# Performance work log

Hardware: AMD Instinct MI355X
Metric: run time of the kernel (lower is better)

Reference implementation:

```python
import jax, jax.numpy as jnp
import numpy as np

P = 3            # spline degree
N_KNOTS = 68     # len(t); K = N_KNOTS - P - 1 = 64
B, D_IN, D_OUT = 4096, 256, 256


def bspline_basis(u, t, p):
    """Vectorized Cox-de Boor recursion.
    u: (N,) evaluation points; t: (n,) sorted knot vector.
    Returns (N, n - p - 1) basis matrix.
    """
    n = t.shape[0]
    uu = u[:, None]                                   # (N, 1)
    # degree-0 indicators over half-open knot intervals: (N, n-1)
    Bmat = ((uu >= t[None, :-1]) & (uu < t[None, 1:])).astype(u.dtype)
    for d in range(1, p + 1):
        ld = t[d:n - 1] - t[:n - d - 1]               # (n-d-1,) left denominators
        rd = t[d + 1:] - t[1:n - d]                   # (n-d-1,) right denominators
        lt = jnp.where(ld > 0, (uu - t[None, :n - d - 1]) / jnp.where(ld > 0, ld, 1.0), 0.0)
        rt = jnp.where(rd > 0, (t[None, d + 1:] - uu) / jnp.where(rd > 0, rd, 1.0), 0.0)
        Bmat = lt * Bmat[:, :-1] + rt * Bmat[:, 1:]
    return Bmat                                        # (N, K)


def setup_inputs() -> dict:
    key = jax.random.key(0)
    k1, k2 = jax.random.split(key)
    K = N_KNOTS - P - 1
    x = jax.random.normal(k1, (B, D_IN), dtype=jnp.float32)
    coeffs = 0.01 * jax.random.normal(k2, (D_OUT, D_IN, K), dtype=jnp.float32)
    mask = jnp.ones((D_OUT, D_IN), dtype=jnp.float32)
    t = jnp.linspace(-4.0, 4.0, N_KNOTS, dtype=jnp.float32)
    return {"x": x, "coeffs": coeffs, "mask": mask, "t": t}


def reference(x, coeffs, mask, t):
    b, d_in = x.shape
    # basis for all (batch, input-dim) points at once -> (B, d_in, K)
    Bx = bspline_basis(x.reshape(-1), t, P).reshape(b, d_in, -1)
    C = coeffs * mask[..., None]                      # (d_out, d_in, K)
    y = jnp.einsum('bik,oik->bo', Bx, C)              # (B, d_out)
    return y
```

## Files before the change

### kernel.cpp

```cpp
#include <hip/hip_runtime.h>

#define NKNOTS 68
#define B_     4096
#define DIN    256
#define DOUT   256
#define KB_    64
#define BM     128
#define BN     128
#define LDA    80
#define KSPLIT 16
#define IPS    (DIN / KSPLIT)

typedef unsigned short ushort_t;
typedef unsigned long long u64_t;
typedef float   f32x4    __attribute__((ext_vector_type(4)));
typedef unsigned int u32x4 __attribute__((ext_vector_type(4)));
typedef ushort_t us16x4  __attribute__((ext_vector_type(4)));
typedef int     int4v    __attribute__((ext_vector_type(4)));

typedef __attribute__((address_space(1))) const unsigned int gu32;
typedef __attribute__((address_space(3))) unsigned int lu32;

__device__ __forceinline__ float bf2f(ushort_t b) {
    union { unsigned u; float f; } c; c.u = ((unsigned)b) << 16; return c.f;
}
__device__ __forceinline__ ushort_t f2bf(float f) {
    union { float f; unsigned u; } c; c.f = f;
    unsigned u = c.u;
    return (ushort_t)((u + 0x7FFFu + ((u >> 16) & 1u)) >> 16);
}
__device__ __forceinline__ bool is_fp32(const void* tkn) {
    return ((*(const unsigned*)tkn) & 0xFFFFu) == 0u;
}

__global__ void kan_prep1(const void* __restrict__ coeffs,
                          const void* __restrict__ mask,
                          const void* __restrict__ x,
                          const void* __restrict__ tkn,
                          unsigned* __restrict__ smax,
                          u64_t* __restrict__ rec64) {
    __shared__ float tt[NKNOTS];
    __shared__ float wmax[4];
    int blk = blockIdx.x;
    int lt  = threadIdx.x;
    bool f32 = is_fp32(tkn);

    if (blk < 2048) {
        int tid = blk * 256 + lt;
        int oi = tid >> 3;
        int o  = tid >> 11;
        int k8 = (tid & 7) * 8;
        size_t base = (size_t)oi * KB_ + k8;
        float v[8], m;
        if (f32) {
            const float* cf = (const float*)coeffs + base;
            f32x4 a = *(const f32x4*)cf;
            f32x4 b = *(const f32x4*)(cf + 4);
            v[0]=a.x; v[1]=a.y; v[2]=a.z; v[3]=a.w; v[4]=b.x; v[5]=b.y; v[6]=b.z; v[7]=b.w;
            m = ((const float*)mask)[oi];
        } else {
            const ushort_t* ch = (const ushort_t*)coeffs + base;
            u32x4 w = *(const u32x4*)ch;
            const ushort_t* h = (const ushort_t*)&w;
            #pragma unroll
            for (int e = 0; e < 8; ++e) v[e] = bf2f(h[e]);
            m = bf2f(((const ushort_t*)mask)[oi]);
        }
        float mx = 0.f;
        #pragma unroll
        for (int e = 0; e < 8; ++e) mx = fmaxf(mx, fabsf(v[e] * m));
        #pragma unroll
        for (int off = 32; off >= 1; off >>= 1)
            mx = fmaxf(mx, __shfl_down(mx, off, 64));
        if ((lt & 63) == 0) wmax[lt >> 6] = mx;
        __syncthreads();
        if (lt == 0) {
            float M = fmaxf(fmaxf(wmax[0], wmax[1]), fmaxf(wmax[2], wmax[3]));
            atomicMax(smax + o, __float_as_uint(M));
        }
    } else {
        if (lt < NKNOTS) tt[lt] = f32 ? ((const float*)tkn)[lt] : bf2f(((const ushort_t*)tkn)[lt]);
        __syncthreads();
        int g = (blk - 2048) * 256 + lt;
        float u = f32 ? ((const float*)x)[g] : bf2f(((const ushort_t*)x)[g]);
        float N0 = 0.f, N1 = 0.f, N2 = 0.f, N3 = 0.f;
        int j = 0;
        bool valid = (u >= tt[0]) && (u < tt[NKNOTS - 1]);
        if (valid) {
            int lo = 0, hi = NKNOTS - 1;
            #pragma unroll
            for (int it = 0; it < 7; ++it) {
                int mid = (lo + hi) >> 1;
                if (u < tt[mid]) hi = mid; else lo = mid;
            }
            j = lo;
            float Nv[4];
            Nv[0] = 1.f; Nv[1] = 0.f; Nv[2] = 0.f; Nv[3] = 0.f;
            #pragma unroll
            for (int d = 1; d <= 3; ++d) {
                float saved = 0.f;
                #pragma unroll
                for (int r = 0; r < 3; ++r) {
                    if (r < d) {
                        int il = j + r + 1 - d;
                        int ir = j + r + 1;
                        il = il < 0 ? 0 : (il > 67 ? 67 : il);
                        ir = ir > 67 ? 67 : ir;
                        float tl = tt[il], tr = tt[ir];
                        float denom = tr - tl;
                        float temp = (denom > 0.f) ? Nv[r] / denom : 0.f;
                        Nv[r] = saved + (tr - u) * temp;
                        saved = (u - tl) * temp;
                    }
                }
                Nv[d] = saved;
            }
            N0 = Nv[0]; N1 = Nv[1]; N2 = Nv[2]; N3 = Nv[3];
        }
        int s = j - 3;
        int sc = s < 0 ? 0 : (s > 60 ? 60 : s);
        unsigned pack = 0;
        #pragma unroll
        for (int r = 0; r < 4; ++r) {
            int rr = (sc + r) - s;
            float v = 0.f;
            v = (rr == 0) ? N0 : v;
            v = (rr == 1) ? N1 : v;
            v = (rr == 2) ? N2 : v;
            v = (rr == 3) ? N3 : v;
            int q = __float2int_rn(127.0f * v);
            pack |= ((unsigned)(q & 0xFF)) << (8 * r);
        }
        rec64[g] = ((u64_t)(unsigned)sc << 32) | pack;
    }
}

__global__ void kan_prep2(const void* __restrict__ coeffs,
                          const void* __restrict__ mask,
                          const void* __restrict__ tkn,
                          const unsigned* __restrict__ smax,
                          signed char* __restrict__ cp8) {
    int tid = blockIdx.x * 256 + threadIdx.x;
    int oi = tid >> 3;
    int o  = tid >> 11;
    int k8 = (tid & 7) * 8;
    size_t base = (size_t)oi * KB_ + k8;
    bool f32 = is_fp32(tkn);
    float maxv = __uint_as_float(smax[o]);
    float sinv = (maxv > 0.f) ? (127.0f / maxv) : 0.f;
    float v[8], m;
    if (f32) {
        const float* cf = (const float*)coeffs + base;
        f32x4 a = *(const f32x4*)cf;
        f32x4 b = *(const f32x4*)(cf + 4);
        v[0]=a.x; v[1]=a.y; v[2]=a.z; v[3]=a.w; v[4]=b.x; v[5]=b.y; v[6]=b.z; v[7]=b.w;
        m = ((const float*)mask)[oi];
    } else {
        const ushort_t* ch = (const ushort_t*)coeffs + base;
        u32x4 w = *(const u32x4*)ch;
        const ushort_t* h = (const ushort_t*)&w;
        #pragma unroll
        for (int e = 0; e < 8; ++e) v[e] = bf2f(h[e]);
        m = bf2f(((const ushort_t*)mask)[oi]);
    }
    u64_t pk = 0;
    #pragma unroll
    for (int e = 0; e < 8; ++e) {
        int q = __float2int_rn(v[e] * m * sinv);
        pk |= ((u64_t)((unsigned)q & 0xFF)) << (8 * e);
    }
    *(u64_t*)(cp8 + base) = pk;
}

__global__ __launch_bounds__(256, 4) void kan_gemm(
    const signed char* __restrict__ cp8,
    const u64_t* __restrict__ rec64,
    const unsigned* __restrict__ smax,
    ushort_t* __restrict__ part)
{
    __shared__ __align__(16) unsigned char As[BM * LDA];
    __shared__ __align__(16) unsigned char Bs[2][BN * KB_];

    int t  = threadIdx.x;
    int bx = blockIdx.x;
    int kt = bx & (KSPLIT - 1);
    int mt = (bx >> 4) & 31;
    int nt = bx >> 9;
    int b0 = mt * BM;
    int o0 = nt * BN;
    int i0 = kt * IPS;

    int wave = t >> 6;
    int lane = t & 63;
    int wm = (wave & 1) * 64;
    int wn = (wave >> 1) * 64;
    int l15 = lane & 15;
    int l4  = lane >> 4;

    #define STAGE(i_, p_)                                                                 \
        {                                                                                 \
            _Pragma("unroll")                                                             \
            for (int j = 0; j < 2; ++j) {                                                 \
                int slot = wave * 128 + j * 64 + lane;                                    \
                int row  = slot >> 2;                                                     \
                int c    = slot & 3;                                                      \
                const signed char* g = cp8 + ((size_t)(o0 + row) * DIN + (i_)) * KB_ + c * 16; \
                lu32* l = (lu32*)(&Bs[p_][(wave * 128 + j * 64) * 16]);                   \
                __builtin_amdgcn_global_load_lds((gu32*)g, l, 16, 0, 0);                  \
            }                                                                             \
        }

    {
        unsigned* As32 = (unsigned*)As;
        #pragma unroll
        for (int j = 0; j < (BM * LDA / 4) / 256; ++j) As32[t + j * 256] = 0u;
    }

    int zrow = t >> 2;
    int zq   = t & 3;
    size_t gb0 = (size_t)(b0 + zrow) * DIN;
    size_t gb1 = (size_t)(b0 + zrow + 64) * DIN;

    STAGE(i0, 0);
    u64_t cur_r0 = rec64[gb0 + i0];
    u64_t cur_r1 = rec64[gb1 + i0];

    int4v acc[4][4];
    #pragma unroll
    for (int a = 0; a < 4; ++a)
        #pragma unroll
        for (int b = 0; b < 4; ++b)
            acc[a][b] = (int4v){0, 0, 0, 0};

    __syncthreads();

    int last0 = 0, last1 = 0;
    u64_t nxt_r0 = 0, nxt_r1 = 0;
    for (int ii = 0; ii < IPS; ++ii) {
        int p = ii & 1;
        int s0 = (int)((cur_r0 >> 32) & 0xFF);
        int s1 = (int)((cur_r1 >> 32) & 0xFF);
        unsigned char v0 = (unsigned char)((cur_r0 >> (8 * zq)) & 0xFF);
        unsigned char v1 = (unsigned char)((cur_r1 >> (8 * zq)) & 0xFF);
        As[zrow * LDA + last0 + zq] = 0;
        As[(zrow + 64) * LDA + last1 + zq] = 0;
        As[zrow * LDA + s0 + zq] = v0;
        As[(zrow + 64) * LDA + s1 + zq] = v1;
        last0 = s0; last1 = s1;
        __syncthreads();
        if (ii + 1 < IPS) {
            int i1 = i0 + ii + 1;
            STAGE(i1, p ^ 1);
            nxt_r0 = rec64[gb0 + i1];
            nxt_r1 = rec64[gb1 + i1];
        }
        int4v af[4], bfr[4];
        #pragma unroll
        for (int a = 0; a < 4; ++a)
            af[a] = *(const int4v*)(&As[(wm + a * 16 + l15) * LDA + l4 * 16]);
        #pragma unroll
        for (int b = 0; b < 4; ++b)
            bfr[b] = *(const int4v*)(&Bs[p][(wn + b * 16 + l15) * KB_ + l4 * 16]);
        #pragma unroll
        for (int a = 0; a < 4; ++a)
            #pragma unroll
            for (int b = 0; b < 4; ++b)
                acc[a][b] = __builtin_amdgcn_mfma_i32_16x16x64_i8(af[a], bfr[b], acc[a][b], 0, 0, 0);
        cur_r0 = nxt_r0; cur_r1 = nxt_r1;
        __syncthreads();
    }

    ushort_t* pout = part + (size_t)kt * (B_ * DOUT);
    float sb[4];
    #pragma unroll
    for (int b = 0; b < 4; ++b) {
        int col = o0 + wn + b * 16 + l15;
        sb[b] = __uint_as_float(smax[col]) * (1.0f / (127.0f * 127.0f));
    }
    #pragma unroll
    for (int a = 0; a < 4; ++a) {
        int row_base = b0 + wm + a * 16 + l4 * 4;
        #pragma unroll
        for (int b = 0; b < 4; ++b) {
            int col = o0 + wn + b * 16 + l15;
            #pragma unroll
            for (int e = 0; e < 4; ++e)
                pout[(size_t)(row_base + e) * DOUT + col] = f2bf((float)acc[a][b][e] * sb[b]);
        }
    }
    #undef STAGE
}

__global__ void kan_reduce(const ushort_t* __restrict__ part,
                           const void* __restrict__ tkn,
                           void* __restrict__ out) {
    int g = blockIdx.x * 256 + threadIdx.x;
    const us16x4* p4 = (const us16x4*)part;
    f32x4 s = (f32x4){0.f, 0.f, 0.f, 0.f};
    #pragma unroll
    for (int kt = 0; kt < KSPLIT; ++kt) {
        us16x4 v = p4[(size_t)kt * (B_ * DOUT / 4) + g];
        s.x += bf2f(v[0]); s.y += bf2f(v[1]); s.z += bf2f(v[2]); s.w += bf2f(v[3]);
    }
    if (is_fp32(tkn)) {
        ((f32x4*)out)[g] = s;
    } else {
        us16x4 o;
        o[0] = f2bf(s.x); o[1] = f2bf(s.y); o[2] = f2bf(s.z); o[3] = f2bf(s.w);
        ((us16x4*)out)[g] = o;
    }
}

extern "C" void kernel_launch(void* const* d_in, const int* in_sizes, int n_in,
                              void* d_out, int out_size, void* d_ws, size_t ws_size,
                              hipStream_t stream) {
    const void* x      = d_in[0];
    const void* coeffs = d_in[1];
    const void* mask   = d_in[2];
    const void* tkn    = d_in[3];

    char* ws = (char*)d_ws;
    signed char* cp8   = (signed char*)(ws);
    u64_t*       rec64 = (u64_t*)(ws + (4u  << 20));
    unsigned*    smax  = (unsigned*)(ws + (12u << 20));
    ushort_t*    part  = (ushort_t*)(ws + (13u << 20));

    hipMemsetAsync(smax, 0, 256 * sizeof(unsigned), stream);
    kan_prep1<<<6144, 256, 0, stream>>>(coeffs, mask, x, tkn, smax, rec64);
    kan_prep2<<<2048, 256, 0, stream>>>(coeffs, mask, tkn, smax, cp8);
    kan_gemm<<<1024, 256, 0, stream>>>(cp8, rec64, smax, part);
    kan_reduce<<<1024, 256, 0, stream>>>(part, tkn, d_out);
}
```

Measured before the change: 121.3 us.

## Halve GEMM K-split, process two input slices per step, drop atomic max

The GEMM now uses 8 K-splits instead of 16, and each block loads two input-dimension slices per pipeline step. This halves the partial-sum buffer written by the GEMM and read by the reduce kernel. B tiles in LDS get a padded stride to reduce bank conflicts, and the rec64 loads are vectorized to fetch two slices at once. The per-output max is no longer built with atomicMax on a memset buffer; each block writes its own max and consumers fold 8 entries. This removes the memset launch and the atomics, at the cost of 512 larger blocks with lower occupancy.

```diff
diff --git a/kernel.cpp b/kernel.cpp
--- a/kernel.cpp
+++ b/kernel.cpp
@@ -7,11 +7,14 @@
 #define KB_    64
 #define BM     128
 #define BN     128
-#define LDA    80
-#define KSPLIT 16
-#define IPS    (DIN / KSPLIT)
+#define LDA    144
+#define LDB    80
+#define KSPLIT 8
+#define IPS    32
+#define NSTEP  16
 
 typedef unsigned short ushort_t;
+typedef unsigned char uchar_t;
 typedef unsigned long long u64_t;
 typedef float   f32x4    __attribute__((ext_vector_type(4)));
 typedef unsigned int u32x4 __attribute__((ext_vector_type(4)));
@@ -37,7 +40,7 @@
                           const void* __restrict__ mask,
                           const void* __restrict__ x,
                           const void* __restrict__ tkn,
-                          unsigned* __restrict__ smax,
+                          float* __restrict__ smax64,
                           u64_t* __restrict__ rec64) {
     __shared__ float tt[NKNOTS];
     __shared__ float wmax[4];
@@ -48,7 +51,6 @@
     if (blk < 2048) {
         int tid = blk * 256 + lt;
         int oi = tid >> 3;
-        int o  = tid >> 11;
         int k8 = (tid & 7) * 8;
         size_t base = (size_t)oi * KB_ + k8;
         float v[8], m;
@@ -74,10 +76,8 @@
             mx = fmaxf(mx, __shfl_down(mx, off, 64));
         if ((lt & 63) == 0) wmax[lt >> 6] = mx;
         __syncthreads();
-        if (lt == 0) {
-            float M = fmaxf(fmaxf(wmax[0], wmax[1]), fmaxf(wmax[2], wmax[3]));
-            atomicMax(smax + o, __float_as_uint(M));
-        }
+        if (lt == 0)
+            smax64[blk] = fmaxf(fmaxf(wmax[0], wmax[1]), fmaxf(wmax[2], wmax[3]));
     } else {
         if (lt < NKNOTS) tt[lt] = f32 ? ((const float*)tkn)[lt] : bf2f(((const ushort_t*)tkn)[lt]);
         __syncthreads();
@@ -138,7 +138,7 @@
 __global__ void kan_prep2(const void* __restrict__ coeffs,
                           const void* __restrict__ mask,
                           const void* __restrict__ tkn,
-                          const unsigned* __restrict__ smax,
+                          const float* __restrict__ smax64,
                           signed char* __restrict__ cp8) {
     int tid = blockIdx.x * 256 + threadIdx.x;
     int oi = tid >> 3;
@@ -146,7 +146,9 @@
     int k8 = (tid & 7) * 8;
     size_t base = (size_t)oi * KB_ + k8;
     bool f32 = is_fp32(tkn);
-    float maxv = __uint_as_float(smax[o]);
+    float maxv = 0.f;
+    #pragma unroll
+    for (int e = 0; e < 8; ++e) maxv = fmaxf(maxv, smax64[(o << 3) + e]);
     float sinv = (maxv > 0.f) ? (127.0f / maxv) : 0.f;
     float v[8], m;
     if (f32) {
@@ -172,20 +174,20 @@
     *(u64_t*)(cp8 + base) = pk;
 }
 
-__global__ __launch_bounds__(256, 4) void kan_gemm(
+__global__ __launch_bounds__(256, 2) void kan_gemm(
     const signed char* __restrict__ cp8,
     const u64_t* __restrict__ rec64,
-    const unsigned* __restrict__ smax,
+    const float* __restrict__ smax64,
     ushort_t* __restrict__ part)
 {
-    __shared__ __align__(16) unsigned char As[BM * LDA];
-    __shared__ __align__(16) unsigned char Bs[2][BN * KB_];
+    __shared__ __align__(16) uchar_t As[BM * LDA];
+    __shared__ __align__(16) uchar_t Bs[2][2 * BN * LDB];
 
     int t  = threadIdx.x;
     int bx = blockIdx.x;
     int kt = bx & (KSPLIT - 1);
-    int mt = (bx >> 4) & 31;
-    int nt = bx >> 9;
+    int mt = (bx >> 3) & 31;
+    int nt = bx >> 8;
     int b0 = mt * BM;
     int o0 = nt * BN;
     int i0 = kt * IPS;
@@ -197,17 +199,27 @@
     int l15 = lane & 15;
     int l4  = lane >> 4;
 
-    #define STAGE(i_, p_)                                                                 \
-        {                                                                                 \
-            _Pragma("unroll")                                                             \
-            for (int j = 0; j < 2; ++j) {                                                 \
-                int slot = wave * 128 + j * 64 + lane;                                    \
-                int row  = slot >> 2;                                                     \
-                int c    = slot & 3;                                                      \
-                const signed char* g = cp8 + ((size_t)(o0 + row) * DIN + (i_)) * KB_ + c * 16; \
-                lu32* l = (lu32*)(&Bs[p_][(wave * 128 + j * 64) * 16]);                   \
-                __builtin_amdgcn_global_load_lds((gu32*)g, l, 16, 0, 0);                  \
-            }                                                                             \
+    size_t gsrc_base[5];
+    unsigned ldsoff[5];
+    #pragma unroll
+    for (int j = 0; j < 5; ++j) {
+        int slot = wave * 320 + j * 64 + lane;
+        int isl  = slot / 640;
+        int w640 = slot - isl * 640;
+        int row  = w640 / 5;
+        int c    = w640 - row * 5;
+        int cc   = (c > 3) ? 3 : c;
+        gsrc_base[j] = ((size_t)(o0 + row) * DIN + isl) * KB_ + cc * 16;
+        ldsoff[j] = (unsigned)((wave * 320 + j * 64) * 16);
+    }
+    #define STAGE(i_, p_)                                                              \
+        {                                                                              \
+            _Pragma("unroll")                                                          \
+            for (int j = 0; j < 5; ++j) {                                              \
+                const signed char* g = cp8 + gsrc_base[j] + (size_t)(i_) * KB_;        \
+                lu32* l = (lu32*)(&Bs[p_][ldsoff[j]]);                                 \
+                __builtin_amdgcn_global_load_lds((gu32*)g, l, 16, 0, 0);               \
+            }                                                                          \
         }
 
     {
@@ -222,8 +234,13 @@
     size_t gb1 = (size_t)(b0 + zrow + 64) * DIN;
 
     STAGE(i0, 0);
-    u64_t cur_r0 = rec64[gb0 + i0];
-    u64_t cur_r1 = rec64[gb1 + i0];
+    u64_t cur_r0[2], cur_r1[2];
+    {
+        u32x4 p0 = *(const u32x4*)(&rec64[gb0 + i0]);
+        u32x4 p1 = *(const u32x4*)(&rec64[gb1 + i0]);
+        cur_r0[0] = ((u64_t)p0.y << 32) | p0.x; cur_r0[1] = ((u64_t)p0.w << 32) | p0.z;
+        cur_r1[0] = ((u64_t)p1.y << 32) | p1.x; cur_r1[1] = ((u64_t)p1.w << 32) | p1.z;
+    }
 
     int4v acc[4][4];
     #pragma unroll
@@ -234,39 +251,50 @@
 
     __syncthreads();
 
-    int last0 = 0, last1 = 0;
-    u64_t nxt_r0 = 0, nxt_r1 = 0;
-    for (int ii = 0; ii < IPS; ++ii) {
-        int p = ii & 1;
-        int s0 = (int)((cur_r0 >> 32) & 0xFF);
-        int s1 = (int)((cur_r1 >> 32) & 0xFF);
-        unsigned char v0 = (unsigned char)((cur_r0 >> (8 * zq)) & 0xFF);
-        unsigned char v1 = (unsigned char)((cur_r1 >> (8 * zq)) & 0xFF);
-        As[zrow * LDA + last0 + zq] = 0;
-        As[(zrow + 64) * LDA + last1 + zq] = 0;
-        As[zrow * LDA + s0 + zq] = v0;
-        As[(zrow + 64) * LDA + s1 + zq] = v1;
-        last0 = s0; last1 = s1;
+    int last0[2] = {0, 0}, last1[2] = {0, 0};
+    u64_t nxt_r0[2] = {0, 0}, nxt_r1[2] = {0, 0};
+    for (int st = 0; st < NSTEP; ++st) {
+        int p = st & 1;
+        #pragma unroll
+        for (int isl = 0; isl < 2; ++isl) {
+            int s0 = (int)((cur_r0[isl] >> 32) & 0xFF);
+            int s1 = (int)((cur_r1[isl] >> 32) & 0xFF);
+            uchar_t v0 = (uchar_t)((cur_r0[isl] >> (8 * zq)) & 0xFF);
+            uchar_t v1 = (uchar_t)((cur_r1[isl] >> (8 * zq)) & 0xFF);
+            As[zrow * LDA + isl * 64 + last0[isl] + zq] = 0;
+            As[(zrow + 64) * LDA + isl * 64 + last1[isl] + zq] = 0;
+            As[zrow * LDA + isl * 64 + s0 + zq] = v0;
+            As[(zrow + 64) * LDA + isl * 64 + s1 + zq] = v1;
+            last0[isl] = s0; last1[isl] = s1;
+        }
         __syncthreads();
-        if (ii + 1 < IPS) {
-            int i1 = i0 + ii + 1;
+        if (st + 1 < NSTEP) {
+            int i1 = i0 + (st + 1) * 2;
             STAGE(i1, p ^ 1);
-            nxt_r0 = rec64[gb0 + i1];
-            nxt_r1 = rec64[gb1 + i1];
-        }
-        int4v af[4], bfr[4];
-        #pragma unroll
-        for (int a = 0; a < 4; ++a)
-            af[a] = *(const int4v*)(&As[(wm + a * 16 + l15) * LDA + l4 * 16]);
-        #pragma unroll
-        for (int b = 0; b < 4; ++b)
-            bfr[b] = *(const int4v*)(&Bs[p][(wn + b * 16 + l15) * KB_ + l4 * 16]);
-        #pragma unroll
-        for (int a = 0; a < 4; ++a)
+            u32x4 p0 = *(const u32x4*)(&rec64[gb0 + i1]);
+            u32x4 p1 = *(const u32x4*)(&rec64[gb1 + i1]);
+            nxt_r0[0] = ((u64_t)p0.y << 32) | p0.x; nxt_r0[1] = ((u64_t)p0.w << 32) | p0.z;
+            nxt_r1[0] = ((u64_t)p1.y << 32) | p1.x; nxt_r1[1] = ((u64_t)p1.w << 32) | p1.z;
+        }
+        #pragma unroll
+        for (int isl = 0; isl < 2; ++isl) {
+            int4v af[4], bfr[4];
+            #pragma unroll
+            for (int a = 0; a < 4; ++a)
+                af[a] = *(const int4v*)(&As[(wm + a * 16 + l15) * LDA + isl * 64 + l4 * 16]);
             #pragma unroll
             for (int b = 0; b < 4; ++b)
-                acc[a][b] = __builtin_amdgcn_mfma_i32_16x16x64_i8(af[a], bfr[b], acc[a][b], 0, 0, 0);
-        cur_r0 = nxt_r0; cur_r1 = nxt_r1;
+                bfr[b] = *(const int4v*)(&Bs[p][isl * (BN * LDB) + (wn + b * 16 + l15) * LDB + l4 * 16]);
+            #pragma unroll
+            for (int a = 0; a < 4; ++a)
+                #pragma unroll
+                for (int b = 0; b < 4; ++b)
+                    acc[a][b] = __builtin_amdgcn_mfma_i32_16x16x64_i8(af[a], bfr[b], acc[a][b], 0, 0, 0);
+        }
+        #pragma unroll
+        for (int isl = 0; isl < 2; ++isl) {
+            cur_r0[isl] = nxt_r0[isl]; cur_r1[isl] = nxt_r1[isl];
+        }
         __syncthreads();
     }
 
@@ -275,7 +303,10 @@
     #pragma unroll
     for (int b = 0; b < 4; ++b) {
         int col = o0 + wn + b * 16 + l15;
-        sb[b] = __uint_as_float(smax[col]) * (1.0f / (127.0f * 127.0f));
+        float mv = 0.f;
+        #pragma unroll
+        for (int e = 0; e < 8; ++e) mv = fmaxf(mv, smax64[(col << 3) + e]);
+        sb[b] = mv * (1.0f / (127.0f * 127.0f));
     }
     #pragma unroll
     for (int a = 0; a < 4; ++a) {
@@ -320,14 +351,13 @@
     const void* tkn    = d_in[3];
 
     char* ws = (char*)d_ws;
-    signed char* cp8   = (signed char*)(ws);
-    u64_t*       rec64 = (u64_t*)(ws + (4u  << 20));
-    unsigned*    smax  = (unsigned*)(ws + (12u << 20));
-    ushort_t*    part  = (ushort_t*)(ws + (13u << 20));
-
-    hipMemsetAsync(smax, 0, 256 * sizeof(unsigned), stream);
-    kan_prep1<<<6144, 256, 0, stream>>>(coeffs, mask, x, tkn, smax, rec64);
-    kan_prep2<<<2048, 256, 0, stream>>>(coeffs, mask, tkn, smax, cp8);
-    kan_gemm<<<1024, 256, 0, stream>>>(cp8, rec64, smax, part);
+    signed char* cp8    = (signed char*)(ws);
+    u64_t*       rec64  = (u64_t*)(ws + (4u  << 20));
+    float*       smax64 = (float*)(ws + (12u << 20));
+    ushort_t*    part   = (ushort_t*)(ws + (13u << 20));
+
+    kan_prep1<<<6144, 256, 0, stream>>>(coeffs, mask, x, tkn, smax64, rec64);
+    kan_prep2<<<2048, 256, 0, stream>>>(coeffs, mask, tkn, smax64, cp8);
+    kan_gemm<<<512, 256, 0, stream>>>(cp8, rec64, smax64, part);
     kan_reduce<<<1024, 256, 0, stream>>>(part, tkn, d_out);
 }
```

Result: faster. 109.2 us (median of 2 runs) (-9.9%).
